# Kernel optimization log

Measured on AMD Instinct MI355X. Metric: run time of the kernel, lower is better.

Reference implementation:

```python
import jax, jax.numpy as jnp
import numpy as np
from jax import lax

WL = 140      # window_length
OFC = 118     # ofc_channel = window_length - 21 - 1
TDN = 21      # TimeDelayNum (sliding time-delay count)
D_CM = 16     # cm_attn embed dim
N_BR = 4      # conv_eeg_audio_number
C_OUT = 10    # conv_output_channel
KS = 9        # conv kernel size

def _init(key, shape, fan_in):
    return jax.random.uniform(key, shape, jnp.float32, -1.0, 1.0) / np.sqrt(fan_in)

def setup_inputs():
    key = jax.random.key(0)
    ks = jax.random.split(key, 12)
    return {
        "x": jax.random.normal(ks[0], (1, 1, 18, WL), dtype=jnp.float32),
        "tdA_in_w": _init(ks[1], (3 * OFC, OFC), OFC),
        "tdA_in_b": jnp.zeros((3 * OFC,), jnp.float32),
        "tdA_out_w": _init(ks[2], (OFC, OFC), OFC),
        "tdA_out_b": jnp.zeros((OFC,), jnp.float32),
        "tdB_in_w": _init(ks[3], (3 * OFC, OFC), OFC),
        "tdB_in_b": jnp.zeros((3 * OFC,), jnp.float32),
        "tdB_out_w": _init(ks[4], (OFC, OFC), OFC),
        "tdB_out_b": jnp.zeros((OFC,), jnp.float32),
        "cm_in_w": _init(ks[5], (N_BR, 3 * D_CM, D_CM), D_CM),
        "cm_in_b": jnp.zeros((N_BR, 3 * D_CM), jnp.float32),
        "cm_out_w": _init(ks[6], (N_BR, D_CM, D_CM), D_CM),
        "cm_out_b": jnp.zeros((N_BR, D_CM), jnp.float32),
        "projA_w": _init(ks[7], (16, 1), 1),
        "projB_w": _init(ks[8], (16, 1), 1),
        "conv_w": _init(ks[9], (N_BR, C_OUT, 16, KS), 16 * KS),
        "conv_b": jnp.zeros((N_BR, C_OUT), jnp.float32),
        "fc1_w": _init(ks[10], (40, 40), 40),
        "fc1_b": jnp.zeros((40,), jnp.float32),
        "fc2_w": _init(ks[11], (2, 40), 40),
        "fc2_b": jnp.zeros((2,), jnp.float32),
    }

def _mha(q, k, v, in_w, in_b, out_w, out_b):
    # single-head attention; q: (Lq, d), k/v: (Lk, d) -> (Lq, d)
    d = q.shape[-1]
    wq, wk, wv = jnp.split(in_w, 3, axis=0)
    bq, bk, bv = jnp.split(in_b, 3)
    qp = (q @ wq.T + bq) * (1.0 / np.sqrt(d))
    kp = k @ wk.T + bk
    vp = v @ wv.T + bv
    attn = jax.nn.softmax(qp @ kp.T, axis=-1)
    return (attn @ vp) @ out_w.T + out_b

def _forward(x, tdA_in_w, tdA_in_b, tdA_out_w, tdA_out_b,
             tdB_in_w, tdB_in_b, tdB_out_w, tdB_out_b,
             cm_in_w, cm_in_b, cm_out_w, cm_out_b,
             projA_w, projB_w, conv_w, conv_b,
             fc1_w, fc1_b, fc2_w, fc2_b):
    sig = x[0, 0]                               # (18, 140)
    wavA_raw, eeg_raw, wavB_raw = sig[0], sig[1:17], sig[17]
    # ChannelWav: sliding time-delay unfold -> (TDN, OFC)
    idx = jnp.arange(TDN)[:, None] + jnp.arange(OFC)[None, :]
    kA = wavA_raw[idx]                          # (21, 118)
    kB = wavB_raw[idx]
    eeg = eeg_raw[:, WL - OFC:]                 # (16, 118)
    # time-delay attention (embed_dim = 118, seq = 16 eeg channels / 21 delays)
    attA = _mha(eeg, kA, kA, tdA_in_w, tdA_in_b, tdA_out_w, tdA_out_b)  # (16, 118)
    attB = _mha(eeg, kB, kB, tdB_in_w, tdB_in_b, tdB_out_w, tdB_out_b)
    # select_max: pick attention row with largest total correlation to eeg
    iA = jnp.argmax(jnp.sum(eeg @ attA.T, axis=1))
    iB = jnp.argmax(jnp.sum(eeg @ attB.T, axis=1))
    wA = projA_w @ attA[iA][None, :]            # 1x1 conv == outer product, (16, 118)
    wB = projB_w @ attB[iB][None, :]
    data = [wA, eeg, eeg, wB]
    kv = [eeg, wA, wB, eeg]
    feats = []
    for i in range(N_BR):                       # 4 structurally distinct branches
        o = _mha(data[i].T, kv[i].T, kv[i].T,
                 cm_in_w[i], cm_in_b[i], cm_out_w[i], cm_out_b[i])      # (118, 16)
        y = lax.conv_general_dilated(o.T[None], conv_w[i], (1,), 'VALID')  # (1, 10, 110)
        y = jax.nn.relu(y[0] + conv_b[i][:, None])
        feats.append(jnp.max(y, axis=-1))       # AdaptiveMaxPool1d(1) -> (10,)
    flat = jnp.concatenate(feats)               # (40,)
    h = jax.nn.sigmoid(flat @ fc1_w.T + fc1_b)
    out = jax.nn.sigmoid(h @ fc2_w.T + fc2_b)
    return out[None, :]                         # (1, 2)

def reference(x, tdA_in_w, tdA_in_b, tdA_out_w, tdA_out_b,
              tdB_in_w, tdB_in_b, tdB_out_w, tdB_out_b,
              cm_in_w, cm_in_b, cm_out_w, cm_out_b,
              projA_w, projB_w, conv_w, conv_b,
              fc1_w, fc1_b, fc2_w, fc2_b):
    return _forward(x, tdA_in_w, tdA_in_b, tdA_out_w, tdA_out_b,
                    tdB_in_w, tdB_in_b, tdB_out_w, tdB_out_b,
                    cm_in_w, cm_in_b, cm_out_w, cm_out_b,
                    projA_w, projB_w, conv_w, conv_b,
                    fc1_w, fc1_b, fc2_w, fc2_b)
```

## Files before the change

### kernel.cpp

```cpp
#include <hip/hip_runtime.h>
#include <math.h>

#define WL   140
#define OFC  118
#define TDN  21
#define COUT 10
#define KS   9
#define IW_SZ (OFC * OFC)

#define PROJ_STRIDE 6848
#define KP_OFF      1888
#define VP_OFF      4368
#define WS_ATT_A    13696
#define WS_ATT_B    13824
#define WS_FEATS    13952
#define WS_FLAGS    14080

#define MAGIC 0x1F2E3D4C
#define NSLOTS 34

struct Params {
    const float *x;
    const float *tdA_in_w, *tdA_in_b, *tdA_out_w, *tdA_out_b;
    const float *tdB_in_w, *tdB_in_b, *tdB_out_w, *tdB_out_b;
    const float *cm_in_w, *cm_in_b, *cm_out_w, *cm_out_b;
    const float *projA_w, *projB_w, *conv_w, *conv_b;
    const float *fc1_w, *fc1_b, *fc2_w, *fc2_b;
    float *fc_unused;
    float *ws, *out;
};

struct TdSm {
    float owpad[OFC][122];
    float qpp[16][122];
    float kpp[TDN][122];
    float vpp[TDN][122];
    float attn[16][22];
    float acs[22];
    float avcs[120];
    float colsum[120];
    float Ssum[16];
    float avsel[120];
    int   sel;
};

struct BrSm {
    float arow[120];
    float pv[16];
    float eeg_s[16][OFC];
    float w_inT[16][48];
    float b_in[48];
    float tv[3][16];
    float w_out[16][16];
    float b_out[16];
    float cw[COUT * 16 * KS];
    float cb[COUT];
    float kpS[OFC][17];
    float vpS[OFC][17];
    float u[120], v2[120];
    float part_m[4][128];
    float part_l[4][128];
    float part_acc[4][OFC][17];
    float o2[OFC][17];
    float qpS[OFC][17];
    float a_[120], dvec[120];
    float Avec[16], Bvec[16];
    float Gc[COUT][KS], cb2[COUT];
    float y[COUT][22];
};

struct HdSm { float f[64]; float h[64]; };

union alignas(16) Sm { TdSm t; BrSm b; HdSm h; };

__device__ inline float wred(float v) {
    #pragma unroll
    for (int off = 32; off; off >>= 1) v += __shfl_xor(v, off);
    return v;
}

__device__ inline void postM(int* f, int tid) {
    __syncthreads();
    if (tid == 0)
        __hip_atomic_store(f, MAGIC, __ATOMIC_RELEASE, __HIP_MEMORY_SCOPE_AGENT);
}

__device__ inline void waitM(int* base, int first, int n, int tid) {
    if (tid == 0) {
        for (int i = 0; i < n; ++i) {
            int* f = base + (first + i) * 16;
            while (__hip_atomic_load(f, __ATOMIC_RELAXED, __HIP_MEMORY_SCOPE_AGENT) != MAGIC)
                __builtin_amdgcn_s_sleep(1);
        }
        __builtin_amdgcn_fence(__ATOMIC_ACQUIRE, "agent");
    }
    __syncthreads();
}

__device__ void td_proj_direct(int side, int lw, int lane, const Params& p)
{
    int sec, o, r, R;
    if (lw < 30) {
        sec = 0; o = lw * 4 + (lane & 3); r = lane >> 2; R = 16;
    } else {
        sec = (lw < 70) ? 1 : 2;
        int base = (lw - (sec == 1 ? 30 : 70)) * 3;
        o = base + lane % 3; r = lane / 3; R = TDN;
    }
    if (o >= OFC || r >= R) return;

    const float* in_w = (side ? p.tdB_in_w : p.tdA_in_w) + sec * IW_SZ + o * OFC;
    const float  bias = (side ? p.tdB_in_b : p.tdA_in_b)[sec * OFC + o];
    const float2* w2  = (const float2*)in_w;
    float s0 = 0.f;

    if (sec == 0) {
        const float2* a = (const float2*)(p.x + (1 + r) * WL + (WL - OFC));
        #pragma unroll 4
        for (int j = 0; j < 59; ++j) {
            float2 u = a[j], w = w2[j];
            s0 += u.x * w.x + u.y * w.y;
        }
        s0 = (s0 + bias) * (1.0f / sqrtf(118.0f));
    } else {
        const float* wr = p.x + (side ? 17 * WL : 0) + r;
        #pragma unroll 4
        for (int j = 0; j < 59; ++j) {
            float2 w = w2[j];
            s0 += wr[2 * j] * w.x + wr[2 * j + 1] * w.y;
        }
        s0 += bias;
    }
    p.ws[side * PROJ_STRIDE
         + (sec == 0 ? 0 : (sec == 1 ? KP_OFF : VP_OFF))
         + r * OFC + o] = s0;
}

__device__ void td_phase2(int b, int tid, const Params& p, TdSm& s)
{
    const float* base  = p.ws + b * PROJ_STRIDE;
    const float* out_b = b ? p.tdB_out_b : p.tdA_out_b;
    const int wid = tid >> 6, lane = tid & 63;

    for (int e = tid; e < 16 * 59; e += 512) {
        int r = e / 59, j = e - r * 59;
        ((float2*)&s.qpp[r][0])[j] = ((const float2*)(base + r * OFC))[j];
    }
    for (int e = tid; e < TDN * 59; e += 512) {
        int t = e / 59, j = e - t * 59;
        ((float2*)&s.kpp[t][0])[j] = ((const float2*)(base + KP_OFF + t * OFC))[j];
        ((float2*)&s.vpp[t][0])[j] = ((const float2*)(base + VP_OFF + t * OFC))[j];
    }
    __syncthreads();

    if (tid < 16 * TDN) {
        int i = tid / TDN, t = tid - (tid / TDN) * TDN;
        const float2* q = (const float2*)&s.qpp[i][0];
        const float2* k = (const float2*)&s.kpp[t][0];
        float sc = 0.f;
        #pragma unroll 4
        for (int j = 0; j < 59; ++j) {
            float2 u = q[j], v = k[j];
            sc += u.x * v.x + u.y * v.y;
        }
        s.attn[i][t] = sc;
    }
    __syncthreads();

    if (tid < 16) {
        float m = s.attn[tid][0];
        for (int t = 1; t < TDN; ++t) m = fmaxf(m, s.attn[tid][t]);
        float l = 0.f;
        for (int t = 0; t < TDN; ++t) {
            float pp = __expf(s.attn[tid][t] - m);
            s.attn[tid][t] = pp;
            l += pp;
        }
        float inv = 1.f / l;
        for (int t = 0; t < TDN; ++t) s.attn[tid][t] *= inv;
    }
    __syncthreads();

    if (tid < TDN) {
        float a = 0.f;
        for (int i = 0; i < 16; ++i) a += s.attn[i][tid];
        s.acs[tid] = a;
    }
    __syncthreads();

    if (tid < OFC) {
        float a = 0.f;
        for (int t = 0; t < TDN; ++t) a += s.acs[t] * s.vpp[t][tid];
        s.avcs[tid] = a;
    }
    __syncthreads();

    if (tid < OFC) {
        const float2* a  = (const float2*)&s.avcs[0];
        const float2* w2 = (const float2*)&s.owpad[tid][0];
        float a0 = 0.f;
        #pragma unroll 4
        for (int j = 0; j < 59; ++j) {
            float2 u = a[j], v = w2[j];
            a0 += u.x * v.x + u.y * v.y;
        }
        s.colsum[tid] = a0 + 16.f * out_b[tid];
    }
    __syncthreads();

    for (int d = wid; d < 16; d += 8) {
        const float* er = p.x + (1 + d) * WL + (WL - OFC);
        int j0 = lane * 2;
        float sc = 0.f;
        if (j0 < OFC) {
            float2 ev = *(const float2*)(er + j0);
            float2 cv = *(const float2*)(&s.colsum[j0]);
            sc = ev.x * cv.x + ev.y * cv.y;
        }
        sc = wred(sc);
        if (lane == 0) s.Ssum[d] = sc;
    }
    __syncthreads();

    if (tid == 0) {
        int best = 0; float bv = s.Ssum[0];
        for (int i = 1; i < 16; ++i)
            if (s.Ssum[i] > bv) { bv = s.Ssum[i]; best = i; }
        s.sel = best;
    }
    __syncthreads();

    if (tid < OFC) {
        float a = 0.f;
        for (int t = 0; t < TDN; ++t) a += s.attn[s.sel][t] * s.vpp[t][tid];
        s.avsel[tid] = a;
    }
    __syncthreads();

    if (tid < OFC) {
        const float2* a  = (const float2*)&s.avsel[0];
        const float2* w2 = (const float2*)&s.owpad[tid][0];
        float a0 = 0.f;
        #pragma unroll 4
        for (int j = 0; j < 59; ++j) {
            float2 u = a[j], v = w2[j];
            a0 += u.x * v.x + u.y * v.y;
        }
        p.ws[(b ? WS_ATT_B : WS_ATT_A) + tid] = a0 + out_b[tid];
    }
}

__device__ void br_pre(int br, int tid, const Params& p, BrSm& s)
{
    const bool d_r1 = (br == 0 || br == 3);

    for (int e = tid; e < 16 * OFC; e += 512) {
        int r = e / OFC, c = e - (e / OFC) * OFC;
        s.eeg_s[r][c] = p.x[(1 + r) * WL + (WL - OFC) + c];
    }
    for (int e = tid; e < 768; e += 512) {
        int q = e / 16, r = e % 16;
        s.w_inT[r][q] = p.cm_in_w[br * 768 + e];
    }
    if (tid < 48) s.b_in[tid] = p.cm_in_b[br * 48 + tid];
    if (tid >= 64 && tid < 320) {
        int e = tid - 64;
        s.w_out[e >> 4][e & 15] = p.cm_out_w[br * 256 + e];
    }
    if (tid >= 384 && tid < 400) s.b_out[tid - 384] = p.cm_out_b[br * 16 + (tid - 384)];
    for (int e = tid; e < COUT * 16 * KS; e += 512) s.cw[e] = p.conv_w[br * 1440 + e];
    if (tid >= 400 && tid < 410) s.cb[tid - 400] = p.conv_b[br * COUT + (tid - 400)];
    {
        const float* pvg = (br < 2) ? p.projA_w : p.projB_w;
        if (tid >= 416 && tid < 432) s.pv[tid - 416] = pvg[tid - 416];
    }
    __syncthreads();

    if (tid < 48) {
        float a = 0.f;
        #pragma unroll
        for (int r = 0; r < 16; ++r) a += s.pv[r] * s.w_inT[r][tid];
        s.tv[tid / 16][tid % 16] = a;
    }
    __syncthreads();

    if (d_r1) {
        for (int e = tid; e < 2 * OFC * 16; e += 512) {
            int sec01 = e / (OFC * 16);
            int rem = e - sec01 * OFC * 16;
            int j = rem >> 4, o = rem & 15;
            float a = 0.f;
            #pragma unroll
            for (int r = 0; r < 16; ++r) a += s.eeg_s[r][j] * s.w_inT[r][(1 + sec01) * 16 + o];
            a += s.b_in[(1 + sec01) * 16 + o];
            (sec01 ? &s.vpS[0][0] : &s.kpS[0][0])[j * 17 + o] = a;
        }
        __syncthreads();
        if (tid < OFC) {
            float uu = 0.f, vv = 0.f;
            #pragma unroll
            for (int o = 0; o < 16; ++o) {
                float kv = s.kpS[tid][o];
                uu += s.tv[0][o] * kv;
                vv += s.b_in[o] * kv;
            }
            s.u[tid] = uu; s.v2[tid] = vv;
        }
    } else {
        for (int e = tid; e < OFC * 16; e += 512) {
            int j = e >> 4, o = e & 15;
            float a = 0.f;
            #pragma unroll
            for (int r = 0; r < 16; ++r) a += s.eeg_s[r][j] * s.w_inT[r][o];
            s.qpS[j][o] = (a + s.b_in[o]) * 0.25f;
        }
        __syncthreads();
        if (tid < OFC) {
            float a = 0.f;
            #pragma unroll
            for (int o = 0; o < 16; ++o) a += s.qpS[tid][o] * s.tv[1][o];
            s.a_[tid] = a;
        }
        if (tid >= 128 && tid < 144) {
            int c = tid - 128;
            float A = 0.f, B = 0.f;
            #pragma unroll
            for (int o = 0; o < 16; ++o) {
                A += s.tv[2][o] * s.w_out[c][o];
                B += s.b_in[32 + o] * s.w_out[c][o];
            }
            s.Avec[c] = A;
            s.Bvec[c] = B + s.b_out[c];
        }
        __syncthreads();
        if (tid < COUT * KS) {
            int c = tid / KS, k = tid - (tid / KS) * KS;
            float g = 0.f;
            #pragma unroll
            for (int m = 0; m < 16; ++m) g += s.Avec[m] * s.cw[(c * 16 + m) * KS + k];
            s.Gc[c][k] = g;
        }
        if (tid >= 128 && tid < 128 + COUT) {
            int c = tid - 128;
            float cc = s.cb[c];
            #pragma unroll
            for (int m = 0; m < 16; ++m) {
                float bsum = 0.f;
                #pragma unroll
                for (int k = 0; k < KS; ++k) bsum += s.cw[(c * 16 + m) * KS + k];
                cc += s.Bvec[m] * bsum;
            }
            s.cb2[c] = cc;
        }
    }
}

__device__ void br_main(int br, int tid, const Params& p, BrSm& s)
{
    const bool d_r1 = (br == 0 || br == 3);
    const float* ar = p.ws + ((br < 2) ? WS_ATT_A : WS_ATT_B);
    if (tid < OFC) s.arow[tid] = ar[tid];
    __syncthreads();

    if (d_r1) {
        const int g = tid >> 7, j = tid & 127;
        float acc[16];
        float m = -INFINITY, l = 0.f;
        #pragma unroll
        for (int r = 0; r < 16; ++r) acc[r] = 0.f;

        if (j < OFC) {
            const float aj = s.arow[j];
            const int t0 = (g * OFC) >> 2, t1 = ((g + 1) * OFC) >> 2;
            for (int t = t0; t < t1; ++t) {
                float sc = 0.25f * fmaf(aj, s.u[t], s.v2[t]);
                float mn = fmaxf(m, sc);
                float c  = __expf(m - mn);
                float pp = __expf(sc - mn);
                l = l * c + pp;
                const float* vr = &s.vpS[t][0];
                #pragma unroll
                for (int r = 0; r < 16; ++r) acc[r] = acc[r] * c + pp * vr[r];
                m = mn;
            }
            s.part_m[g][j] = m;
            s.part_l[g][j] = l;
            #pragma unroll
            for (int r = 0; r < 16; ++r) s.part_acc[g][j][r] = acc[r];
        }
        __syncthreads();

        if (tid < OFC) {
            float m0 = s.part_m[0][tid], m1 = s.part_m[1][tid];
            float m2 = s.part_m[2][tid], m3 = s.part_m[3][tid];
            float mm = fmaxf(fmaxf(m0, m1), fmaxf(m2, m3));
            float c0 = __expf(m0 - mm), c1 = __expf(m1 - mm);
            float c2 = __expf(m2 - mm), c3 = __expf(m3 - mm);
            float ll = c0 * s.part_l[0][tid] + c1 * s.part_l[1][tid]
                     + c2 * s.part_l[2][tid] + c3 * s.part_l[3][tid];
            float inv = 1.f / ll;
            float orow[16];
            #pragma unroll
            for (int r = 0; r < 16; ++r)
                orow[r] = (c0 * s.part_acc[0][tid][r] + c1 * s.part_acc[1][tid][r]
                         + c2 * s.part_acc[2][tid][r] + c3 * s.part_acc[3][tid][r]) * inv;
            for (int c = 0; c < 16; ++c) {
                float a = s.b_out[c];
                #pragma unroll
                for (int d = 0; d < 16; ++d) a += orow[d] * s.w_out[c][d];
                s.o2[tid][c] = a;
            }
        }
        __syncthreads();

        if (tid < COUT * 22) {
            int c = tid / 22, grp = tid - (tid / 22) * 22;
            int pbase = grp * 5;
            float acc5[5];
            #pragma unroll
            for (int i = 0; i < 5; ++i) acc5[i] = s.cb[c];
            for (int mI = 0; mI < 16; ++mI) {
                float win[13];
                #pragma unroll
                for (int t = 0; t < 13; ++t) win[t] = s.o2[pbase + t][mI];
                #pragma unroll
                for (int k = 0; k < KS; ++k) {
                    float wv = s.cw[(c * 16 + mI) * KS + k];
                    #pragma unroll
                    for (int i = 0; i < 5; ++i) acc5[i] += win[i + k] * wv;
                }
            }
            float mx = fmaxf(fmaxf(fmaxf(acc5[0], acc5[1]), fmaxf(acc5[2], acc5[3])), acc5[4]);
            s.y[c][grp] = fmaxf(mx, 0.f);
        }
        __syncthreads();
    } else {
        if (tid < OFC) {
            const float aj = s.a_[tid];
            float m = -INFINITY;
            for (int t = 0; t < OFC; ++t) m = fmaxf(m, aj * s.arow[t]);
            float l = 0.f, d = 0.f;
            for (int t = 0; t < OFC; ++t) {
                float e = __expf(aj * s.arow[t] - m);
                l += e;
                d += e * s.arow[t];
            }
            s.dvec[tid] = d / l;
        }
        __syncthreads();

        if (tid < COUT * 22) {
            int c = tid / 22, grp = tid - (tid / 22) * 22;
            int pbase = grp * 5;
            float win[13];
            #pragma unroll
            for (int t = 0; t < 13; ++t) win[t] = s.dvec[pbase + t];
            float acc5[5];
            #pragma unroll
            for (int i = 0; i < 5; ++i) acc5[i] = s.cb2[c];
            #pragma unroll
            for (int k = 0; k < KS; ++k) {
                float wv = s.Gc[c][k];
                #pragma unroll
                for (int i = 0; i < 5; ++i) acc5[i] += win[i + k] * wv;
            }
            float mx = fmaxf(fmaxf(fmaxf(acc5[0], acc5[1]), fmaxf(acc5[2], acc5[3])), acc5[4]);
            s.y[c][grp] = fmaxf(mx, 0.f);
        }
        __syncthreads();
    }

    if (tid < COUT) {
        float mx = s.y[tid][0];
        for (int g2 = 1; g2 < 22; ++g2) mx = fmaxf(mx, s.y[tid][g2]);
        p.ws[WS_FEATS + br * COUT + tid] = mx;
    }
}

__global__ __launch_bounds__(512) void fused_net(Params p)
{
    __shared__ Sm sm;
    const int blk = blockIdx.x;
    const int tid = threadIdx.x;
    int* flags = (int*)(p.ws + WS_FLAGS);

    if (blk >= 2 && blk < 30) {
        const int side = (blk < 16) ? 0 : 1;
        const int gw   = (blk - (side ? 16 : 2)) * 8 + (tid >> 6);
        if (gw < 110) td_proj_direct(side, gw, tid & 63, p);
        postM(&flags[(blk - 2) * 16], tid);
        return;
    }

    if (blk < 2) {
        const float* ow = blk ? p.tdB_out_w : p.tdA_out_w;
        for (int e = tid; e < OFC * 59; e += 512) {
            int o = e / 59, j = e - o * 59;
            ((float2*)&sm.t.owpad[o][0])[j] = ((const float2*)(ow + o * OFC))[j];
        }
        waitM(flags, blk ? 14 : 0, 14, tid);
        td_phase2(blk, tid, p, sm.t);
        postM(&flags[(28 + blk) * 16], tid);

        if (blk == 0) {
            waitM(flags, 30, 4, tid);
            if (tid < NSLOTS)
                __hip_atomic_store(&flags[tid * 16], 0,
                                   __ATOMIC_RELAXED, __HIP_MEMORY_SCOPE_AGENT);
            __syncthreads();
            if (tid < 40) sm.h.f[tid] = p.ws[WS_FEATS + tid];
            __syncthreads();
            if (tid < 40) {
                float a = p.fc1_b[tid];
                for (int k = 0; k < 40; ++k) a += sm.h.f[k] * p.fc1_w[tid * 40 + k];
                sm.h.h[tid] = 1.f / (1.f + __expf(-a));
            }
            __syncthreads();
            if (tid < 2) {
                float a = p.fc2_b[tid];
                for (int k = 0; k < 40; ++k) a += sm.h.h[k] * p.fc2_w[tid * 40 + k];
                p.out[tid] = 1.f / (1.f + __expf(-a));
            }
        }
        return;
    }

    const int br = blk - 30;
    br_pre(br, tid, p, sm.b);
    waitM(flags, (br < 2) ? 28 : 29, 1, tid);
    br_main(br, tid, p, sm.b);
    postM(&flags[(30 + br) * 16], tid);
}

extern "C" void kernel_launch(void* const* d_in, const int* in_sizes, int n_in,
                              void* d_out, int out_size, void* d_ws, size_t ws_size,
                              hipStream_t stream) {
    Params prm;
    prm.x         = (const float*)d_in[0];
    prm.tdA_in_w  = (const float*)d_in[1];
    prm.tdA_in_b  = (const float*)d_in[2];
    prm.tdA_out_w = (const float*)d_in[3];
    prm.tdA_out_b = (const float*)d_in[4];
    prm.tdB_in_w  = (const float*)d_in[5];
    prm.tdB_in_b  = (const float*)d_in[6];
    prm.tdB_out_w = (const float*)d_in[7];
    prm.tdB_out_b = (const float*)d_in[8];
    prm.cm_in_w   = (const float*)d_in[9];
    prm.cm_in_b   = (const float*)d_in[10];
    prm.cm_out_w  = (const float*)d_in[11];
    prm.cm_out_b  = (const float*)d_in[12];
    prm.projA_w   = (const float*)d_in[13];
    prm.projB_w   = (const float*)d_in[14];
    prm.conv_w    = (const float*)d_in[15];
    prm.conv_b    = (const float*)d_in[16];
    prm.fc1_w     = (const float*)d_in[17];
    prm.fc1_b     = (const float*)d_in[18];
    prm.fc2_w     = (const float*)d_in[19];
    prm.fc2_b     = (const float*)d_in[20];
    prm.fc_unused = nullptr;
    prm.ws        = (float*)d_ws;
    prm.out       = (float*)d_out;

    fused_net<<<dim3(34), dim3(512), 0, stream>>>(prm);
}
```

Measured before the change: 39.75 us.

## Move V projection into main blocks and prefold output weights before waiting

The V projection of each time-delay attention now runs inside the two main blocks, and V is pre-multiplied by the output weight matrix while those blocks wait for the Q/K projection blocks. Once the Q/K results arrive, this collapses two dependent matvec stages into a single 21-term reduction. Softmax becomes a wave-shuffle reduction across rows. EEG rows and the FC head weights are staged in shared memory. Grid drops from 34 to 24 blocks, which shortens the critical path but gives the main blocks more serial work (about 2.5k dot products of length 118) before the barrier.

Measured after the change: 71.49 us. +79.8%, slower.

```diff
diff --git a/kernel.cpp b/kernel.cpp
--- a/kernel.cpp
+++ b/kernel.cpp
@@ -10,14 +10,13 @@
 
 #define PROJ_STRIDE 6848
 #define KP_OFF      1888
-#define VP_OFF      4368
 #define WS_ATT_A    13696
 #define WS_ATT_B    13824
 #define WS_FEATS    13952
 #define WS_FLAGS    14080
 
 #define MAGIC 0x1F2E3D4C
-#define NSLOTS 34
+#define NSLOTS 24
 
 struct Params {
     const float *x;
@@ -26,21 +25,23 @@
     const float *cm_in_w, *cm_in_b, *cm_out_w, *cm_out_b;
     const float *projA_w, *projB_w, *conv_w, *conv_b;
     const float *fc1_w, *fc1_b, *fc2_w, *fc2_b;
-    float *fc_unused;
     float *ws, *out;
 };
 
-struct TdSm {
-    float owpad[OFC][122];
+struct MnSm {
+    float wout[OFC][122];
+    float vp [TDN][122];
+    float vpw[TDN][122];
     float qpp[16][122];
     float kpp[TDN][122];
-    float vpp[TDN][122];
+    float eeg[16][122];
     float attn[16][22];
     float acs[22];
-    float avcs[120];
     float colsum[120];
     float Ssum[16];
-    float avsel[120];
+    float bout[120];
+    float fc1w[1600], fc1b[40], fc2w[80], fc2b[2];
+    float hf[40], hh[40];
     int   sel;
 };
 
@@ -69,9 +70,7 @@
     float y[COUT][22];
 };
 
-struct HdSm { float f[64]; float h[64]; };
-
-union alignas(16) Sm { TdSm t; BrSm b; HdSm h; };
+union alignas(16) Sm { MnSm m; BrSm b; };
 
 __device__ inline float wred(float v) {
     #pragma unroll
@@ -97,16 +96,11 @@
     __syncthreads();
 }
 
-__device__ void td_proj_direct(int side, int lw, int lane, const Params& p)
+__device__ void qk_task(int side, int lw, int lane, const Params& p)
 {
     int sec, o, r, R;
-    if (lw < 30) {
-        sec = 0; o = lw * 4 + (lane & 3); r = lane >> 2; R = 16;
-    } else {
-        sec = (lw < 70) ? 1 : 2;
-        int base = (lw - (sec == 1 ? 30 : 70)) * 3;
-        o = base + lane % 3; r = lane / 3; R = TDN;
-    }
+    if (lw < 30) { sec = 0; o = lw * 4 + (lane & 3); r = lane >> 2; R = 16; }
+    else         { sec = 1; o = (lw - 30) * 3 + lane % 3; r = lane / 3; R = TDN; }
     if (o >= OFC || r >= R) return;
 
     const float* in_w = (side ? p.tdB_in_w : p.tdA_in_w) + sec * IW_SZ + o * OFC;
@@ -131,17 +125,70 @@
         }
         s0 += bias;
     }
-    p.ws[side * PROJ_STRIDE
-         + (sec == 0 ? 0 : (sec == 1 ? KP_OFF : VP_OFF))
-         + r * OFC + o] = s0;
-}
-
-__device__ void td_phase2(int b, int tid, const Params& p, TdSm& s)
+    p.ws[side * PROJ_STRIDE + (sec == 0 ? 0 : KP_OFF) + r * OFC + o] = s0;
+}
+
+__device__ void main_block(int b, int tid, const Params& p, MnSm& s)
 {
-    const float* base  = p.ws + b * PROJ_STRIDE;
-    const float* out_b = b ? p.tdB_out_b : p.tdA_out_b;
     const int wid = tid >> 6, lane = tid & 63;
-
+    int* flags = (int*)(p.ws + WS_FLAGS);
+
+    const float* ow = b ? p.tdB_out_w : p.tdA_out_w;
+    for (int e = tid; e < OFC * 59; e += 512) {
+        int o = e / 59, j = e - o * 59;
+        ((float2*)&s.wout[o][0])[j] = ((const float2*)(ow + o * OFC))[j];
+    }
+    for (int e = tid; e < 16 * OFC; e += 512) {
+        int r = e / OFC, c = e - (e / OFC) * OFC;
+        s.eeg[r][c] = p.x[(1 + r) * WL + (WL - OFC) + c];
+    }
+    if (tid < OFC) s.bout[tid] = (b ? p.tdB_out_b : p.tdA_out_b)[tid];
+    if (b == 0) {
+        for (int e = tid; e < 1600; e += 512) s.fc1w[e] = p.fc1_w[e];
+        if (tid < 40) s.fc1b[tid] = p.fc1_b[tid];
+        if (tid >= 64 && tid < 144) s.fc2w[tid - 64] = p.fc2_w[tid - 64];
+        if (tid >= 160 && tid < 162) s.fc2b[tid - 160] = p.fc2_b[tid - 160];
+    }
+
+    {
+        const float* in_w = (b ? p.tdB_in_w : p.tdA_in_w) + 2 * IW_SZ;
+        const float* in_b = (b ? p.tdB_in_b : p.tdA_in_b) + 2 * OFC;
+        const float* wav  = p.x + (b ? 17 * WL : 0);
+        for (int rd = 0; rd < 5; ++rd) {
+            int task = rd * 8 + wid;
+            if (task < 40) {
+                int o = task * 3 + lane % 3, r = lane / 3;
+                if (o < OFC && r < TDN) {
+                    const float2* w2 = (const float2*)(in_w + o * OFC);
+                    const float* wr = wav + r;
+                    float s0 = 0.f;
+                    #pragma unroll 4
+                    for (int j = 0; j < 59; ++j) {
+                        float2 w = w2[j];
+                        s0 += wr[2 * j] * w.x + wr[2 * j + 1] * w.y;
+                    }
+                    s.vp[r][o] = s0 + in_b[o];
+                }
+            }
+        }
+    }
+    __syncthreads();
+
+    for (int e = tid; e < TDN * OFC; e += 512) {
+        int t = e / OFC, j = e - t * OFC;
+        const float2* a  = (const float2*)&s.vp[t][0];
+        const float2* w2 = (const float2*)&s.wout[j][0];
+        float acc = 0.f;
+        #pragma unroll 4
+        for (int oo = 0; oo < 59; ++oo) {
+            float2 u = a[oo], w = w2[oo];
+            acc += u.x * w.x + u.y * w.y;
+        }
+        s.vpw[t][j] = acc;
+    }
+
+    waitM(flags, b * 9, 9, tid);
+    const float* base = p.ws + b * PROJ_STRIDE;
     for (int e = tid; e < 16 * 59; e += 512) {
         int r = e / 59, j = e - r * 59;
         ((float2*)&s.qpp[r][0])[j] = ((const float2*)(base + r * OFC))[j];
@@ -149,7 +196,6 @@
     for (int e = tid; e < TDN * 59; e += 512) {
         int t = e / 59, j = e - t * 59;
         ((float2*)&s.kpp[t][0])[j] = ((const float2*)(base + KP_OFF + t * OFC))[j];
-        ((float2*)&s.vpp[t][0])[j] = ((const float2*)(base + VP_OFF + t * OFC))[j];
     }
     __syncthreads();
 
@@ -167,17 +213,18 @@
     }
     __syncthreads();
 
-    if (tid < 16) {
-        float m = s.attn[tid][0];
-        for (int t = 1; t < TDN; ++t) m = fmaxf(m, s.attn[tid][t]);
-        float l = 0.f;
-        for (int t = 0; t < TDN; ++t) {
-            float pp = __expf(s.attn[tid][t] - m);
-            s.attn[tid][t] = pp;
-            l += pp;
-        }
-        float inv = 1.f / l;
-        for (int t = 0; t < TDN; ++t) s.attn[tid][t] *= inv;
+    {
+        int row = wid * 2 + (lane >= 32 ? 1 : 0);
+        int t   = lane & 31;
+        float v = (t < TDN) ? s.attn[row][t] : -INFINITY;
+        float m = v;
+        #pragma unroll
+        for (int off = 16; off; off >>= 1) m = fmaxf(m, __shfl_xor(m, off, 32));
+        float pp = (t < TDN) ? __expf(v - m) : 0.f;
+        float l = pp;
+        #pragma unroll
+        for (int off = 16; off; off >>= 1) l += __shfl_xor(l, off, 32);
+        if (t < TDN) s.attn[row][t] = pp / l;
     }
     __syncthreads();
 
@@ -190,30 +237,17 @@
 
     if (tid < OFC) {
         float a = 0.f;
-        for (int t = 0; t < TDN; ++t) a += s.acs[t] * s.vpp[t][tid];
-        s.avcs[tid] = a;
-    }
-    __syncthreads();
-
-    if (tid < OFC) {
-        const float2* a  = (const float2*)&s.avcs[0];
-        const float2* w2 = (const float2*)&s.owpad[tid][0];
-        float a0 = 0.f;
-        #pragma unroll 4
-        for (int j = 0; j < 59; ++j) {
-            float2 u = a[j], v = w2[j];
-            a0 += u.x * v.x + u.y * v.y;
-        }
-        s.colsum[tid] = a0 + 16.f * out_b[tid];
+        #pragma unroll 3
+        for (int t = 0; t < TDN; ++t) a += s.acs[t] * s.vpw[t][tid];
+        s.colsum[tid] = a + 16.f * s.bout[tid];
     }
     __syncthreads();
 
     for (int d = wid; d < 16; d += 8) {
-        const float* er = p.x + (1 + d) * WL + (WL - OFC);
         int j0 = lane * 2;
         float sc = 0.f;
         if (j0 < OFC) {
-            float2 ev = *(const float2*)(er + j0);
+            float2 ev = *(const float2*)(&s.eeg[d][j0]);
             float2 cv = *(const float2*)(&s.colsum[j0]);
             sc = ev.x * cv.x + ev.y * cv.y;
         }
@@ -232,21 +266,30 @@
 
     if (tid < OFC) {
         float a = 0.f;
-        for (int t = 0; t < TDN; ++t) a += s.attn[s.sel][t] * s.vpp[t][tid];
-        s.avsel[tid] = a;
-    }
-    __syncthreads();
-
-    if (tid < OFC) {
-        const float2* a  = (const float2*)&s.avsel[0];
-        const float2* w2 = (const float2*)&s.owpad[tid][0];
-        float a0 = 0.f;
-        #pragma unroll 4
-        for (int j = 0; j < 59; ++j) {
-            float2 u = a[j], v = w2[j];
-            a0 += u.x * v.x + u.y * v.y;
-        }
-        p.ws[(b ? WS_ATT_B : WS_ATT_A) + tid] = a0 + out_b[tid];
+        #pragma unroll 3
+        for (int t = 0; t < TDN; ++t) a += s.attn[s.sel][t] * s.vpw[t][tid];
+        p.ws[(b ? WS_ATT_B : WS_ATT_A) + tid] = a + s.bout[tid];
+    }
+    postM(&flags[(18 + b) * 16], tid);
+
+    if (b == 0) {
+        waitM(flags, 20, 4, tid);
+        if (tid < NSLOTS)
+            __hip_atomic_store(&flags[tid * 16], 0,
+                               __ATOMIC_RELAXED, __HIP_MEMORY_SCOPE_AGENT);
+        if (tid < 40) s.hf[tid] = p.ws[WS_FEATS + tid];
+        __syncthreads();
+        if (tid < 40) {
+            float a = s.fc1b[tid];
+            for (int k = 0; k < 40; ++k) a += s.hf[k] * s.fc1w[tid * 40 + k];
+            s.hh[tid] = 1.f / (1.f + __expf(-a));
+        }
+        __syncthreads();
+        if (tid < 2) {
+            float a = s.fc2b[tid];
+            for (int k = 0; k < 40; ++k) a += s.hh[k] * s.fc2w[tid * 40 + k];
+            p.out[tid] = 1.f / (1.f + __expf(-a));
+        }
     }
 }
 
@@ -484,52 +527,24 @@
     const int tid = threadIdx.x;
     int* flags = (int*)(p.ws + WS_FLAGS);
 
-    if (blk >= 2 && blk < 30) {
-        const int side = (blk < 16) ? 0 : 1;
-        const int gw   = (blk - (side ? 16 : 2)) * 8 + (tid >> 6);
-        if (gw < 110) td_proj_direct(side, gw, tid & 63, p);
+    if (blk >= 2 && blk < 20) {
+        const int side = (blk < 11) ? 0 : 1;
+        const int gw   = (blk - (side ? 11 : 2)) * 8 + (tid >> 6);
+        if (gw < 70) qk_task(side, gw, tid & 63, p);
         postM(&flags[(blk - 2) * 16], tid);
         return;
     }
 
     if (blk < 2) {
-        const float* ow = blk ? p.tdB_out_w : p.tdA_out_w;
-        for (int e = tid; e < OFC * 59; e += 512) {
-            int o = e / 59, j = e - o * 59;
-            ((float2*)&sm.t.owpad[o][0])[j] = ((const float2*)(ow + o * OFC))[j];
-        }
-        waitM(flags, blk ? 14 : 0, 14, tid);
-        td_phase2(blk, tid, p, sm.t);
-        postM(&flags[(28 + blk) * 16], tid);
-
-        if (blk == 0) {
-            waitM(flags, 30, 4, tid);
-            if (tid < NSLOTS)
-                __hip_atomic_store(&flags[tid * 16], 0,
-                                   __ATOMIC_RELAXED, __HIP_MEMORY_SCOPE_AGENT);
-            __syncthreads();
-            if (tid < 40) sm.h.f[tid] = p.ws[WS_FEATS + tid];
-            __syncthreads();
-            if (tid < 40) {
-                float a = p.fc1_b[tid];
-                for (int k = 0; k < 40; ++k) a += sm.h.f[k] * p.fc1_w[tid * 40 + k];
-                sm.h.h[tid] = 1.f / (1.f + __expf(-a));
-            }
-            __syncthreads();
-            if (tid < 2) {
-                float a = p.fc2_b[tid];
-                for (int k = 0; k < 40; ++k) a += sm.h.h[k] * p.fc2_w[tid * 40 + k];
-                p.out[tid] = 1.f / (1.f + __expf(-a));
-            }
-        }
+        main_block(blk, tid, p, sm.m);
         return;
     }
 
-    const int br = blk - 30;
+    const int br = blk - 20;
     br_pre(br, tid, p, sm.b);
-    waitM(flags, (br < 2) ? 28 : 29, 1, tid);
+    waitM(flags, (br < 2) ? 18 : 19, 1, tid);
     br_main(br, tid, p, sm.b);
-    postM(&flags[(30 + br) * 16], tid);
+    postM(&flags[(20 + br) * 16], tid);
 }
 
 extern "C" void kernel_launch(void* const* d_in, const int* in_sizes, int n_in,
@@ -557,9 +572,8 @@
     prm.fc1_b     = (const float*)d_in[18];
     prm.fc2_w     = (const float*)d_in[19];
     prm.fc2_b     = (const float*)d_in[20];
-    prm.fc_unused = nullptr;
     prm.ws        = (float*)d_ws;
     prm.out       = (float*)d_out;
 
-    fused_net<<<dim3(34), dim3(512), 0, stream>>>(prm);
-}
+    fused_net<<<dim3(24), dim3(512), 0, stream>>>(prm);
+}
```
